# Performance work log

Measured on AMD Instinct MI355X. Metric: run time of the kernel, lower is better.

Reference implementation:

```python
import jax, jax.numpy as jnp
import numpy as np

LAG = 5
MSG_HID = 256
N_ATOMS = 30
N_EDGES = N_ATOMS * (N_ATOMS - 1)  # 870
BATCH = 2
T = 200


def _rel_matrices():
    # fully-connected directed graph, no self loops (standard NRI encoding)
    recv, send = [], []
    for i in range(N_ATOMS):
        for j in range(N_ATOMS):
            if i != j:
                recv.append(i)
                send.append(j)
    rel_rec = np.zeros((N_EDGES, N_ATOMS), dtype=np.float32)
    rel_send = np.zeros((N_EDGES, N_ATOMS), dtype=np.float32)
    rel_rec[np.arange(N_EDGES), recv] = 1.0
    rel_send[np.arange(N_EDGES), send] = 1.0
    return jnp.asarray(rel_rec), jnp.asarray(rel_send)


def setup_inputs() -> dict:
    key = jax.random.key(0)
    ks = jax.random.split(key, 14)
    rel_rec, rel_send = _rel_matrices()
    s = 0.05
    return {
        "inputs": jax.random.normal(ks[0], (BATCH, N_ATOMS, T), jnp.float32),
        "mu": jax.random.normal(ks[1], (BATCH, N_EDGES), jnp.float32),
        "logvar": jax.random.normal(ks[2], (BATCH, N_EDGES), jnp.float32) * 0.1,
        "eps": jax.random.normal(ks[3], (BATCH, N_EDGES), jnp.float32),
        "rel_rec": rel_rec,
        "rel_send": rel_send,
        "w_msg1": jax.random.normal(ks[4], (2 * LAG, MSG_HID), jnp.float32) * s,
        "b_msg1": jnp.zeros((MSG_HID,), jnp.float32),
        "w_msg2": jax.random.normal(ks[5], (MSG_HID, MSG_HID), jnp.float32) * s,
        "b_msg2": jnp.zeros((MSG_HID,), jnp.float32),
        "w_out1": jax.random.normal(ks[6], (LAG + MSG_HID, MSG_HID), jnp.float32) * s,
        "b_out1": jnp.zeros((MSG_HID,), jnp.float32),
        "w_out2": jax.random.normal(ks[7], (MSG_HID, MSG_HID), jnp.float32) * s,
        "b_out2": jnp.zeros((MSG_HID,), jnp.float32),
        "w_out3": jax.random.normal(ks[8], (MSG_HID, 1), jnp.float32) * s,
        "b_out3": jnp.zeros((1,), jnp.float32),
    }


def reference(inputs, mu, logvar, eps, rel_rec, rel_send,
              w_msg1, b_msg1, w_msg2, b_msg2,
              w_out1, b_out1, w_out2, b_out2, w_out3, b_out3):
    # reparametrize: edges [B, E]
    edges = eps * jnp.exp(0.5 * logvar) + mu

    # lag-stack: data [B, T-lag, N, lag]
    Tm = inputs.shape[2] - LAG
    data = jnp.stack([inputs[:, :, i:i + Tm] for i in range(LAG)], axis=-1)
    data = jnp.transpose(data, (0, 2, 1, 3))  # [B, Tm, N, lag]

    # gather node features to edges via one-hot matmuls
    receivers = jnp.einsum('en,btnl->btel', rel_rec, data)   # [B, Tm, E, lag]
    senders = jnp.einsum('en,btnl->btel', rel_send, data)    # [B, Tm, E, lag]
    pre_msg = jnp.concatenate([senders, receivers], axis=-1)  # [B, Tm, E, 2*lag]

    msg = jax.nn.relu(pre_msg @ w_msg1 + b_msg1)
    msg = jax.nn.relu(msg @ w_msg2 + b_msg2)                 # [B, Tm, E, hid]
    msg = msg * edges[:, None, :, None]                       # edge mask

    # scatter-aggregate messages back to receiver nodes
    agg_msgs = jnp.einsum('bteh,en->btnh', msg, rel_rec)      # [B, Tm, N, hid]

    aug = jnp.concatenate([data, agg_msgs], axis=-1)          # [B, Tm, N, lag+hid]
    pred = jax.nn.relu(aug @ w_out1 + b_out1)
    pred = jax.nn.relu(pred @ w_out2 + b_out2)
    pred = (pred @ w_out3 + b_out3)[..., 0]                   # [B, Tm, N]

    return jnp.transpose(pred, (0, 2, 1))                     # [B, N, Tm]
```

## Files before the change

### kernel.cpp

```cpp
#include <hip/hip_runtime.h>

#define LAG 5
#define HID 256
#define NA 30
#define NE 870
#define TM 195
#define TT 200
#define NB 2
#define EPN 29
#define TB3 65
#define NROWS (NB * TM * NA)
#define APAD 4
#define KC 32
#define UVB 1463
#define W2F_ELEMS (HID * HID)
#define W1F_ELEMS (HID * 288)
#define NWG2 (NB * NA * TB3)
#define Q8 (NWG2 / 8)
#define R8 (NWG2 % 8)

typedef _Float16 f16;
typedef _Float16 f16x8 __attribute__((ext_vector_type(8)));
typedef float floatx4 __attribute__((ext_vector_type(4)));
typedef float floatx16 __attribute__((ext_vector_type(16)));

__global__ __launch_bounds__(256) void k1_prep(
    const float* __restrict__ inputs, const float* __restrict__ w_msg1,
    const float* __restrict__ b_msg1, const float* __restrict__ w_msg2,
    const float* __restrict__ w_out1, const float* __restrict__ w_out2,
    f16* __restrict__ u, f16* __restrict__ v, f16* __restrict__ w2frag,
    f16* __restrict__ w1frag, f16* __restrict__ w2ofrag)
{
    const int bid = blockIdx.x, tid = threadIdx.x;
    if (bid < UVB) {
        __shared__ float feats8[8][LAG];
        const int r0 = bid * 8;
        if (tid < 8 * LAG) {
            const int i = tid / LAG, l = tid % LAG;
            const int r = r0 + i;
            float fv = 0.f;
            if (r < NROWS) {
                const int b = r / (TM * NA), rem = r % (TM * NA);
                const int t = rem / NA, n = rem % NA;
                fv = inputs[(b * NA + n) * TT + t + l];
            }
            feats8[i][l] = fv;
        }
        float w1c[2 * LAG];
        #pragma unroll
        for (int k = 0; k < 2 * LAG; ++k) w1c[k] = w_msg1[k * HID + tid];
        const float bb = b_msg1[tid];
        __syncthreads();
        #pragma unroll
        for (int i = 0; i < 8; ++i) {
            const int r = r0 + i;
            if (r < NROWS) {
                float ua = bb, va = 0.f;
                #pragma unroll
                for (int l = 0; l < LAG; ++l) {
                    ua = fmaf(feats8[i][l], w1c[l], ua);
                    va = fmaf(feats8[i][l], w1c[LAG + l], va);
                }
                u[(r << 8) + tid] = (f16)ua;
                v[(r << 8) + tid] = (f16)va;
            }
        }
    } else if (bid < UVB + 32) {
        const int fidx = (bid - UVB) * 256 + tid;
        const int lane = fidx & 63;
        const int kc = (fidx >> 6) & 15;
        const int c32 = fidx >> 10;
        const int col = c32 * 32 + (lane & 31);
        const int kb = kc * 16 + (lane >> 5) * 8;
        f16x8 vv;
        #pragma unroll
        for (int x = 0; x < 8; ++x) vv[x] = (f16)w_msg2[(kb + x) * HID + col];
        *(f16x8*)&w2frag[fidx * 8] = vv;
    } else if (bid < UVB + 32 + 36) {
        const int fidx = (bid - (UVB + 32)) * 256 + tid;
        const int lane = fidx & 63;
        const int kc = (fidx >> 6) % 9;
        const int ntc = fidx / (64 * 9);
        const int col = ntc * 16 + (lane & 15);
        const int kb = kc * KC + (lane >> 4) * 8;
        f16x8 vv;
        #pragma unroll
        for (int x = 0; x < 8; ++x) {
            const int k = kb + x;
            float val;
            if (k < 256)      val = w_out1[(5 + k) * HID + col];
            else if (k < 261) val = w_out1[(k - 256) * HID + col];
            else              val = 0.f;
            vv[x] = (f16)val;
        }
        *(f16x8*)&w1frag[fidx * 8] = vv;
    } else {
        const int fidx = (bid - (UVB + 32 + 36)) * 256 + tid;
        const int lane = fidx & 63;
        const int kc = (fidx >> 6) & 7;
        const int ntc = fidx >> 9;
        const int col = ntc * 16 + (lane & 15);
        const int kb = kc * KC + (lane >> 4) * 8;
        f16x8 vv;
        #pragma unroll
        for (int x = 0; x < 8; ++x) vv[x] = (f16)w_out2[(kb + x) * HID + col];
        *(f16x8*)&w2ofrag[fidx * 8] = vv;
    }
}

__global__ __launch_bounds__(512, 4) void k2_msg(
    const f16* __restrict__ u, const f16* __restrict__ v,
    const f16* __restrict__ w2frag,
    const float* __restrict__ mu, const float* __restrict__ logvar,
    const float* __restrict__ eps, const float* __restrict__ b_msg2,
    f16* __restrict__ agg)
{
    __shared__ f16 a_lds[96 * 256];
    __shared__ float ev_lds[32];

    const int bid0 = blockIdx.x;
    const int xcd = bid0 & 7, sub = bid0 >> 3;
    const int bid = (xcd < R8 ? xcd * (Q8 + 1) : R8 * (Q8 + 1) + (xcd - R8) * Q8) + sub;

    const int n  = bid % NA;
    const int tb = (bid / NA) % TB3;
    const int b  = bid / (NA * TB3);
    const int t0 = tb * 3;
    const int tid = threadIdx.x;
    const int lane = tid & 63, w = tid >> 6;
    const int h = lane >> 5, l31 = lane & 31;

    if (tid < 32) {
        float evv = 0.f;
        if (tid < EPN) {
            const int e = b * NE + n * EPN + tid;
            evv = eps[e] * __expf(0.5f * logvar[e]) + mu[e];
        }
        ev_lds[tid] = evv;
    }

    const f16x8 z8 = {(f16)0, (f16)0, (f16)0, (f16)0, (f16)0, (f16)0, (f16)0, (f16)0};

    const int sbase = (b * TM + t0) * NA;
    #pragma unroll
    for (int i = 0; i < 6; ++i) {
        const int task = i * 512 + tid;
        const int row = task >> 5, c = task & 31;
        const int tt = row >> 5, ei = row & 31;
        f16x8 out8 = z8;
        if (ei < EPN) {
            const int j = ei + (ei >= n);
            const f16x8 uu = *(const f16x8*)(u + (((sbase + tt * NA + j) << 8) + c * 8));
            const f16x8 vv = *(const f16x8*)(v + (((sbase + tt * NA + n) << 8) + c * 8));
            out8 = __builtin_elementwise_max(uu + vv, z8);
        }
        *(f16x8*)&a_lds[row * 256 + ((c * 8) ^ ((row & 7) << 3))] = out8;
    }

    const f16* bbase = w2frag + ((w * 16) << 9) + (lane << 3);
    f16x8 b0 = *(const f16x8*)(bbase + (0 << 9));
    f16x8 b1 = *(const f16x8*)(bbase + (1 << 9));

    floatx16 acc[3];
    #pragma unroll
    for (int mt = 0; mt < 3; ++mt)
        #pragma unroll
        for (int x = 0; x < 16; ++x) acc[mt][x] = 0.f;

    __syncthreads();

    #pragma unroll
    for (int kc = 0; kc < 16; ++kc) {
        f16x8 b2 = b1;
        if (kc < 14) b2 = *(const f16x8*)(bbase + ((kc + 2) << 9));
        f16x8 af[3];
        #pragma unroll
        for (int mt = 0; mt < 3; ++mt) {
            const int row = mt * 32 + l31;
            af[mt] = *(const f16x8*)&a_lds[row * 256 + ((kc * 16 + h * 8) ^ ((row & 7) << 3))];
        }
        __builtin_amdgcn_s_setprio(1);
        #pragma unroll
        for (int mt = 0; mt < 3; ++mt)
            acc[mt] = __builtin_amdgcn_mfma_f32_32x32x16_f16(af[mt], b0, acc[mt], 0, 0, 0);
        __builtin_amdgcn_s_setprio(0);
        b0 = b1; b1 = b2;
    }

    float evr[16];
    #pragma unroll
    for (int reg = 0; reg < 16; ++reg)
        evr[reg] = ev_lds[(reg & 3) + 8 * (reg >> 2) + 4 * h];
    const float b2s = b_msg2[w * 32 + l31];

    #pragma unroll
    for (int mt = 0; mt < 3; ++mt) {
        const int t = t0 + mt;
        float part = 0.f;
        #pragma unroll
        for (int reg = 0; reg < 16; ++reg)
            part += evr[reg] * fmaxf(acc[mt][reg] + b2s, 0.f);
        part += __shfl_xor(part, 32, 64);
        if (h == 0)
            agg[(((b * TM + t) * NA + n) << 8) + w * 32 + l31] = (f16)part;
    }
}

__global__ __launch_bounds__(256) void k3_out(
    const f16* __restrict__ agg, const float* __restrict__ inputs,
    const f16* __restrict__ w1frag, const f16* __restrict__ w2ofrag,
    const float* __restrict__ b_out1, const float* __restrict__ b_out2,
    const float* __restrict__ w_out3, const float* __restrict__ b_out3,
    float* __restrict__ out)
{
    __shared__ f16 a1[16][288 + APAD];
    __shared__ float red[4][16];

    const int R0 = blockIdx.x * 16;
    const int tid = threadIdx.x;
    const int lane = tid & 63, w = tid >> 6;
    const int q = lane >> 4, m15 = lane & 15;
    const int wbase = w * 64;

    #pragma unroll
    for (int i = 0; i < 2; ++i) {
        const int task = i * 256 + tid;
        const int row = task >> 5, c = task & 31;
        const int R = R0 + row;
        f16x8 val;
        if (R < NROWS) {
            val = *(const f16x8*)&agg[(R << 8) + c * 8];
        } else {
            for (int x = 0; x < 8; ++x) val[x] = (f16)0.f;
        }
        *(f16x8*)&a1[row][c * 8] = val;
    }
    if (tid < 16) {
        const int R = R0 + tid;
        if (R < NROWS) {
            const int b = R / (TM * NA), rem = R % (TM * NA);
            const int t = rem / NA, n = rem % NA;
            const float* ip = inputs + (b * NA + n) * TT + t;
            #pragma unroll
            for (int l = 0; l < LAG; ++l) a1[tid][256 + l] = (f16)ip[l];
            #pragma unroll
            for (int k = 261; k < 288; ++k) a1[tid][k] = (f16)0.f;
        } else {
            for (int k = 256; k < 288; ++k) a1[tid][k] = (f16)0.f;
        }
    }

    floatx4 acc[4];
    #pragma unroll
    for (int nt = 0; nt < 4; ++nt) acc[nt] = (floatx4){0.f, 0.f, 0.f, 0.f};

    const f16* b1base = w1frag + (lane << 3);
    f16x8 bcur[4], bnxt[4];
    #pragma unroll
    for (int nt = 0; nt < 4; ++nt)
        bcur[nt] = *(const f16x8*)(b1base + (((w * 4 + nt) * 9 + 0) << 9));

    __syncthreads();

    #pragma unroll
    for (int kc = 0; kc < 9; ++kc) {
        if (kc < 8) {
            #pragma unroll
            for (int nt = 0; nt < 4; ++nt)
                bnxt[nt] = *(const f16x8*)(b1base + (((w * 4 + nt) * 9 + kc + 1) << 9));
        }
        const f16x8 af = *(const f16x8*)&a1[m15][kc * KC + q * 8];
        #pragma unroll
        for (int nt = 0; nt < 4; ++nt)
            acc[nt] = __builtin_amdgcn_mfma_f32_16x16x32_f16(af, bcur[nt], acc[nt], 0, 0, 0);
        #pragma unroll
        for (int nt = 0; nt < 4; ++nt) bcur[nt] = bnxt[nt];
    }
    __syncthreads();

    {
        float b1v[4];
        #pragma unroll
        for (int nt = 0; nt < 4; ++nt) b1v[nt] = b_out1[wbase + nt * 16 + m15];
        #pragma unroll
        for (int nt = 0; nt < 4; ++nt)
            #pragma unroll
            for (int reg = 0; reg < 4; ++reg)
                a1[q * 4 + reg][wbase + nt * 16 + m15] =
                    (f16)fmaxf(acc[nt][reg] + b1v[nt], 0.f);
    }

    #pragma unroll
    for (int nt = 0; nt < 4; ++nt) acc[nt] = (floatx4){0.f, 0.f, 0.f, 0.f};

    const f16* b2base = w2ofrag + (lane << 3);
    #pragma unroll
    for (int nt = 0; nt < 4; ++nt)
        bcur[nt] = *(const f16x8*)(b2base + (((w * 4 + nt) * 8 + 0) << 9));

    __syncthreads();

    #pragma unroll
    for (int kc = 0; kc < 8; ++kc) {
        if (kc < 7) {
            #pragma unroll
            for (int nt = 0; nt < 4; ++nt)
                bnxt[nt] = *(const f16x8*)(b2base + (((w * 4 + nt) * 8 + kc + 1) << 9));
        }
        const f16x8 af = *(const f16x8*)&a1[m15][kc * KC + q * 8];
        #pragma unroll
        for (int nt = 0; nt < 4; ++nt)
            acc[nt] = __builtin_amdgcn_mfma_f32_16x16x32_f16(af, bcur[nt], acc[nt], 0, 0, 0);
        #pragma unroll
        for (int nt = 0; nt < 4; ++nt) bcur[nt] = bnxt[nt];
    }

    {
        float b2v[4], w3v[4];
        #pragma unroll
        for (int nt = 0; nt < 4; ++nt) {
            const int col = wbase + nt * 16 + m15;
            b2v[nt] = b_out2[col];
            w3v[nt] = w_out3[col];
        }
        #pragma unroll
        for (int reg = 0; reg < 4; ++reg) {
            float p = 0.f;
            #pragma unroll
            for (int nt = 0; nt < 4; ++nt)
                p += fmaxf(acc[nt][reg] + b2v[nt], 0.f) * w3v[nt];
            p += __shfl_xor(p, 1, 64);
            p += __shfl_xor(p, 2, 64);
            p += __shfl_xor(p, 4, 64);
            p += __shfl_xor(p, 8, 64);
            if (m15 == 0) red[w][q * 4 + reg] = p;
        }
    }
    __syncthreads();
    if (tid < 16) {
        const int R = R0 + tid;
        if (R < NROWS) {
            const float val = red[0][tid] + red[1][tid] + red[2][tid] + red[3][tid] + b_out3[0];
            const int b = R / (TM * NA), rem = R % (TM * NA);
            const int t = rem / NA, n = rem % NA;
            out[(b * NA + n) * TM + t] = val;
        }
    }
}

extern "C" void kernel_launch(void* const* d_in, const int* in_sizes, int n_in,
                              void* d_out, int out_size, void* d_ws, size_t ws_size,
                              hipStream_t stream) {
    const float* inputs  = (const float*)d_in[0];
    const float* mu      = (const float*)d_in[1];
    const float* logvar  = (const float*)d_in[2];
    const float* eps     = (const float*)d_in[3];
    const float* w_msg1  = (const float*)d_in[6];
    const float* b_msg1  = (const float*)d_in[7];
    const float* w_msg2  = (const float*)d_in[8];
    const float* b_msg2  = (const float*)d_in[9];
    const float* w_out1  = (const float*)d_in[10];
    const float* b_out1  = (const float*)d_in[11];
    const float* w_out2  = (const float*)d_in[12];
    const float* b_out2  = (const float*)d_in[13];
    const float* w_out3  = (const float*)d_in[14];
    const float* b_out3  = (const float*)d_in[15];
    float* out = (float*)d_out;

    f16* u       = (f16*)d_ws;
    f16* v       = u       + NROWS * HID;
    f16* aggw    = v       + NROWS * HID;
    f16* w2frag  = aggw    + NROWS * HID;
    f16* w1frag  = w2frag  + W2F_ELEMS;
    f16* w2ofrag = w1frag  + W1F_ELEMS;

    hipLaunchKernelGGL(k1_prep, dim3(UVB + 32 + 36 + 32), dim3(256), 0, stream,
                       inputs, w_msg1, b_msg1, w_msg2, w_out1, w_out2,
                       u, v, w2frag, w1frag, w2ofrag);
    hipLaunchKernelGGL(k2_msg, dim3(NWG2), dim3(512), 0, stream,
                       u, v, w2frag, mu, logvar, eps, b_msg2, aggw);
    hipLaunchKernelGGL(k3_out, dim3((NROWS + 15) / 16), dim3(256), 0, stream,
                       aggw, inputs, w1frag, w2ofrag, b_out1, b_out2, w_out3, b_out3, out);
}
```

Measured before the change: 165.1 us.

## Reorder u/v as chunk-major node layout and store A in fragment order

k1 now writes the u/v activations as [b, t, 8-wide channel chunk, node, 8], so each 8-wide chunk of all 30 nodes is contiguous. k2 fills LDS directly in MFMA-fragment order, so each lane's A fragment is a linear 16-byte read and the XOR swizzle goes away. The prefetch of w2 B-fragments from global memory is deepened from two stages to three. In exchange, k1's stores are more scattered (stride 240 per chunk), and the B prefetch holds more registers.

```diff
diff --git a/kernel.cpp b/kernel.cpp
--- a/kernel.cpp
+++ b/kernel.cpp
@@ -51,6 +51,7 @@
         for (int k = 0; k < 2 * LAG; ++k) w1c[k] = w_msg1[k * HID + tid];
         const float bb = b_msg1[tid];
         __syncthreads();
+        const int c = tid >> 3, e = tid & 7;
         #pragma unroll
         for (int i = 0; i < 8; ++i) {
             const int r = r0 + i;
@@ -61,8 +62,11 @@
                     ua = fmaf(feats8[i][l], w1c[l], ua);
                     va = fmaf(feats8[i][l], w1c[LAG + l], va);
                 }
-                u[(r << 8) + tid] = (f16)ua;
-                v[(r << 8) + tid] = (f16)va;
+                const int b = r / (TM * NA), rem = r % (TM * NA);
+                const int t = rem / NA, n = rem % NA;
+                const int base = ((b * TM + t) * 32 + c) * 240 + n * 8 + e;
+                u[base] = (f16)ua;
+                v[base] = (f16)va;
             }
         }
     } else if (bid < UVB + 32) {
@@ -115,7 +119,7 @@
     const float* __restrict__ eps, const float* __restrict__ b_msg2,
     f16* __restrict__ agg)
 {
-    __shared__ f16 a_lds[96 * 256];
+    __shared__ f16 a_lds[48 * 64 * 8];
     __shared__ float ev_lds[32];
 
     const int bid0 = blockIdx.x;
@@ -141,25 +145,28 @@
 
     const f16x8 z8 = {(f16)0, (f16)0, (f16)0, (f16)0, (f16)0, (f16)0, (f16)0, (f16)0};
 
-    const int sbase = (b * TM + t0) * NA;
     #pragma unroll
     for (int i = 0; i < 6; ++i) {
         const int task = i * 512 + tid;
-        const int row = task >> 5, c = task & 31;
-        const int tt = row >> 5, ei = row & 31;
+        const int frag = task >> 6, fl = task & 63;
+        const int tt = frag >> 4, kc = frag & 15;
+        const int hh = fl >> 5, ei = fl & 31;
+        const int c = kc * 2 + hh;
+        const int rowbase = ((b * TM + t0 + tt) * 32 + c) * 240;
         f16x8 out8 = z8;
         if (ei < EPN) {
             const int j = ei + (ei >= n);
-            const f16x8 uu = *(const f16x8*)(u + (((sbase + tt * NA + j) << 8) + c * 8));
-            const f16x8 vv = *(const f16x8*)(v + (((sbase + tt * NA + n) << 8) + c * 8));
+            const f16x8 uu = *(const f16x8*)(u + rowbase + j * 8);
+            const f16x8 vv = *(const f16x8*)(v + rowbase + n * 8);
             out8 = __builtin_elementwise_max(uu + vv, z8);
         }
-        *(f16x8*)&a_lds[row * 256 + ((c * 8) ^ ((row & 7) << 3))] = out8;
+        *(f16x8*)&a_lds[task * 8] = out8;
     }
 
     const f16* bbase = w2frag + ((w * 16) << 9) + (lane << 3);
     f16x8 b0 = *(const f16x8*)(bbase + (0 << 9));
     f16x8 b1 = *(const f16x8*)(bbase + (1 << 9));
+    f16x8 b2 = *(const f16x8*)(bbase + (2 << 9));
 
     floatx16 acc[3];
     #pragma unroll
@@ -171,20 +178,18 @@
 
     #pragma unroll
     for (int kc = 0; kc < 16; ++kc) {
-        f16x8 b2 = b1;
-        if (kc < 14) b2 = *(const f16x8*)(bbase + ((kc + 2) << 9));
+        f16x8 b3 = b2;
+        if (kc < 13) b3 = *(const f16x8*)(bbase + ((kc + 3) << 9));
         f16x8 af[3];
         #pragma unroll
-        for (int mt = 0; mt < 3; ++mt) {
-            const int row = mt * 32 + l31;
-            af[mt] = *(const f16x8*)&a_lds[row * 256 + ((kc * 16 + h * 8) ^ ((row & 7) << 3))];
-        }
+        for (int mt = 0; mt < 3; ++mt)
+            af[mt] = *(const f16x8*)&a_lds[((mt * 16 + kc) * 64 + lane) * 8];
         __builtin_amdgcn_s_setprio(1);
         #pragma unroll
         for (int mt = 0; mt < 3; ++mt)
             acc[mt] = __builtin_amdgcn_mfma_f32_32x32x16_f16(af[mt], b0, acc[mt], 0, 0, 0);
         __builtin_amdgcn_s_setprio(0);
-        b0 = b1; b1 = b2;
+        b0 = b1; b1 = b2; b2 = b3;
     }
 
     float evr[16];
```

New measurement: 163.1 us. Within noise of the previous version (-1.2%).
